# Kernel tuning notes

Hardware: AMD Instinct MI355X
Metric: run time of the kernel (lower is better)

Reference implementation:

```python
import jax, jax.numpy as jnp
import numpy as np

D_MODEL = 1024
NUM_HEADS = 16
HEAD_DIM = D_MODEL // NUM_HEADS


def setup_inputs() -> dict:
    key = jax.random.key(0)
    ks = jax.random.split(key, 5)
    x = jax.random.normal(ks[0], (4, 2048, D_MODEL), dtype=jnp.float32)
    # xavier_uniform with gain=0.1 for square (D,D) weights: limit = 0.1*sqrt(6/(D+D))
    limit = 0.1 * np.sqrt(6.0 / (2 * D_MODEL))
    def w(k):
        return jax.random.uniform(k, (D_MODEL, D_MODEL), jnp.float32, -limit, limit)
    return {
        "x": x,
        "W_q": w(ks[1]), "b_q": jnp.zeros((D_MODEL,), jnp.float32),
        "W_k": w(ks[2]), "b_k": jnp.zeros((D_MODEL,), jnp.float32),
        "W_v": w(ks[3]), "b_v": jnp.zeros((D_MODEL,), jnp.float32),
        "W_o": w(ks[4]), "b_o": jnp.zeros((D_MODEL,), jnp.float32),
    }


def reference(x, W_q, b_q, W_k, b_k, W_v, b_v, W_o, b_o):
    B, S, D = x.shape
    H, Hd = NUM_HEADS, HEAD_DIM
    # Linear: x @ W^T + b (torch nn.Linear convention); weights here are (out, in)
    def proj(W, b):
        y = jnp.einsum('bsd,ed->bse', x, W) + b
        return y.reshape(B, S, H, Hd).transpose(0, 2, 1, 3)  # [B,H,S,Hd]
    Q = proj(W_q, b_q)
    K = proj(W_k, b_k)
    V = proj(W_v, b_v)
    scale = 1.0 / np.sqrt(Hd).astype(np.float32)
    scores = jnp.einsum('bhqd,bhkd->bhqk', Q, K) * scale  # [B,H,S,S]
    attn = jax.nn.softmax(scores, axis=-1)
    ctx = jnp.einsum('bhqk,bhkd->bhqd', attn, V)
    ctx = ctx.transpose(0, 2, 1, 3).reshape(B, S, D)
    out = jnp.einsum('bsd,ed->bse', ctx, W_o) + b_o
    return out
```

## Files before the change

### kernel.cpp

```cpp
#include <hip/hip_runtime.h>
#include <math.h>

#define B_  4
#define S_  2048
#define D_  1024
#define H_  16
#define HD_ 64
#define M_  (B_*S_)

typedef short short8 __attribute__((ext_vector_type(8)));
typedef float f32x4 __attribute__((ext_vector_type(4)));

#define MFMA16(a,b,c) __builtin_amdgcn_mfma_f32_16x16x32_bf16(a, b, c, 0, 0, 0)

#if __has_builtin(__builtin_amdgcn_exp2f)
#define EXP2(x) __builtin_amdgcn_exp2f(x)
#else
#define EXP2(x) exp2f(x)
#endif

__device__ __forceinline__ unsigned short f2bf(float f) {
    unsigned u = __float_as_uint(f);
    u = (u + 0x7FFF + ((u >> 16) & 1)) >> 16;
    return (unsigned short)u;
}

__device__ __forceinline__ unsigned pack_bf16(float a, float b) {
#if __has_builtin(__builtin_amdgcn_cvt_pk_bf16_f32)
    typedef __bf16 bf2 __attribute__((ext_vector_type(2)));
    bf2 v = __builtin_amdgcn_cvt_pk_bf16_f32(a, b);
    unsigned r;
    __builtin_memcpy(&r, &v, 4);
    return r;
#else
    unsigned ua = __float_as_uint(a), ub = __float_as_uint(b);
    ua += 0x7FFFu + ((ua >> 16) & 1u);
    ub += 0x7FFFu + ((ub >> 16) & 1u);
    return __builtin_amdgcn_perm(ub, ua, 0x07060302u);
#endif
}

__device__ __forceinline__ void async_copy16(const void* g, void* l) {
    __builtin_amdgcn_global_load_lds(
        (const __attribute__((address_space(1))) void*)g,
        (__attribute__((address_space(3))) void*)l, 16, 0, 0);
}

__global__ __launch_bounds__(256) void cvt_all(
    const float* __restrict__ x,
    const float* __restrict__ w0, const float* __restrict__ w1,
    const float* __restrict__ w2, const float* __restrict__ w3,
    unsigned short* __restrict__ xb, unsigned short* __restrict__ wb)
{
    size_t i = ((size_t)blockIdx.x * 256 + threadIdx.x) * 4;
    const float* src; unsigned short* dst;
    if (i < (size_t)M_ * D_) {
        src = x + i; dst = xb + i;
    } else {
        size_t j = i - (size_t)M_ * D_;
        int z = (int)(j >> 20);
        const float* w = (z == 0) ? w0 : (z == 1) ? w1 : (z == 2) ? w2 : w3;
        src = w + (j & ((size_t)D_ * D_ - 1)); dst = wb + j;
    }
    float4 v = *(const float4*)src;
    uint2 o;
    o.x = pack_bf16(v.x, v.y);
    o.y = pack_bf16(v.z, v.w);
    *(uint2*)dst = o;
}

__global__ __launch_bounds__(512, 2) void qkv8(
    const unsigned short* __restrict__ A,
    const unsigned short* __restrict__ W,
    const float* __restrict__ bq, const float* __restrict__ bk,
    const float* __restrict__ bv,
    unsigned short* __restrict__ Qo, unsigned short* __restrict__ Ko,
    unsigned short* __restrict__ Vo)
{
    __shared__ unsigned short As[2][256 * 64];
    __shared__ unsigned short Ws[2][256 * 64];
    const int K = D_;
    int tid = threadIdx.x;
    int w = tid >> 6, lane = tid & 63;
    int quad = lane >> 4, l16 = lane & 15;
    int r8 = lane >> 3, c8 = lane & 7;
    int cK = c8 ^ r8;
    int wm = w >> 2, wn = w & 3;

    int lin = blockIdx.x + 12 * blockIdx.y;
    int swz = (lin & 7) * 48 + (lin >> 3);
    int by = swz / 12, bx = swz % 12;
    int m0 = by * 256, n0 = bx * 256;
    int fl = l16 & 7;

    int z = n0 >> 10;
    const float* bias = (z == 0) ? bq : (z == 1) ? bk : bv;
    unsigned short* out = (z == 0) ? Qo : (z == 1) ? Ko : Vo;
    float cscale = (z == 0) ? 0.125f * 1.44269504088896f : 1.0f;

    f32x4 acc[8][4];
    #pragma unroll
    for (int i = 0; i < 8; ++i)
        #pragma unroll
        for (int j = 0; j < 4; ++j)
            acc[i][j] = (f32x4){0.f, 0.f, 0.f, 0.f};

    const unsigned short* Ag = A + (size_t)(m0 + w * 8 + r8) * K + cK * 8;
    const unsigned short* Wg = W + (size_t)(n0 + w * 8 + r8) * K + cK * 8;

    auto stageA = [&](int slot, int kt) {
        #pragma unroll
        for (int ii = 0; ii < 4; ++ii)
            async_copy16(Ag + (size_t)(ii * 64) * K + kt * 64,
                         &As[slot][(ii * 64 + w * 8) * 64]);
    };
    auto stageW = [&](int slot, int kt) {
        #pragma unroll
        for (int ii = 0; ii < 4; ++ii)
            async_copy16(Wg + (size_t)(ii * 64) * K + kt * 64,
                         &Ws[slot][(ii * 64 + w * 8) * 64]);
    };

    stageA(0, 0);
    stageW(0, 0);
    __syncthreads();

    #define RDA(cur, i, s) (*(const short8*)&As[cur][(wm * 128 + (i) * 16 + l16) * 64 + \
                             (((quad + (s) * 4) ^ fl) * 8)])
    #define RDB(cur, j, s) (*(const short8*)&Ws[cur][(wn * 64 + (j) * 16 + l16) * 64 + \
                             (((quad + (s) * 4) ^ fl) * 8)])

    for (int kt = 0; kt < 16; ++kt) {
        int cur = kt & 1;
        bool pre = (kt < 15);
        short8 a[4][2], b0[2][2], b1[2][2];

        #pragma unroll
        for (int i = 0; i < 4; ++i)
            #pragma unroll
            for (int s = 0; s < 2; ++s) a[i][s] = RDA(cur, i, s);
        #pragma unroll
        for (int j = 0; j < 2; ++j)
            #pragma unroll
            for (int s = 0; s < 2; ++s) b0[j][s] = RDB(cur, j, s);
        if (pre) stageA(cur ^ 1, kt + 1);
        __builtin_amdgcn_s_setprio(1);
        #pragma unroll
        for (int i = 0; i < 4; ++i)
            #pragma unroll
            for (int j = 0; j < 2; ++j)
                #pragma unroll
                for (int s = 0; s < 2; ++s)
                    acc[i][j] = MFMA16(a[i][s], b0[j][s], acc[i][j]);
        __builtin_amdgcn_s_setprio(0);
        __builtin_amdgcn_s_barrier();
        __builtin_amdgcn_sched_barrier(0);

        #pragma unroll
        for (int j = 0; j < 2; ++j)
            #pragma unroll
            for (int s = 0; s < 2; ++s) b1[j][s] = RDB(cur, j + 2, s);
        if (pre) stageW(cur ^ 1, kt + 1);
        __builtin_amdgcn_s_setprio(1);
        #pragma unroll
        for (int i = 0; i < 4; ++i)
            #pragma unroll
            for (int j = 0; j < 2; ++j)
                #pragma unroll
                for (int s = 0; s < 2; ++s)
                    acc[i][j + 2] = MFMA16(a[i][s], b1[j][s], acc[i][j + 2]);
        __builtin_amdgcn_s_setprio(0);
        __builtin_amdgcn_s_barrier();
        __builtin_amdgcn_sched_barrier(0);

        #pragma unroll
        for (int i = 0; i < 4; ++i)
            #pragma unroll
            for (int s = 0; s < 2; ++s) a[i][s] = RDA(cur, i + 4, s);
        __builtin_amdgcn_s_setprio(1);
        #pragma unroll
        for (int i = 0; i < 4; ++i)
            #pragma unroll
            for (int j = 0; j < 2; ++j)
                #pragma unroll
                for (int s = 0; s < 2; ++s)
                    acc[i + 4][j + 2] = MFMA16(a[i][s], b1[j][s], acc[i + 4][j + 2]);
        __builtin_amdgcn_s_setprio(0);
        __builtin_amdgcn_s_barrier();
        __builtin_amdgcn_sched_barrier(0);

        __builtin_amdgcn_s_setprio(1);
        #pragma unroll
        for (int i = 0; i < 4; ++i)
            #pragma unroll
            for (int j = 0; j < 2; ++j)
                #pragma unroll
                for (int s = 0; s < 2; ++s)
                    acc[i + 4][j] = MFMA16(a[i][s], b0[j][s], acc[i + 4][j]);
        __builtin_amdgcn_s_setprio(0);
        asm volatile("s_waitcnt vmcnt(0)" ::: "memory");
        __builtin_amdgcn_s_barrier();
        __builtin_amdgcn_sched_barrier(0);
    }
    #undef RDA
    #undef RDB

    #pragma unroll
    for (int i = 0; i < 8; ++i) {
        int mb = m0 + wm * 128 + i * 16 + quad * 4;
        #pragma unroll
        for (int j = 0; j < 4; ++j) {
            int n = n0 + wn * 64 + j * 16 + l16;
            int nn = n & 1023;
            float bn = bias[nn];
            int h = nn >> 6, hd = nn & 63;
            if (z != 2) {
                #pragma unroll
                for (int r = 0; r < 4; ++r) {
                    int m = mb + r;
                    int bb = m >> 11, s = m & (S_ - 1);
                    out[(((size_t)(bb * H_ + h)) * S_ + s) * HD_ + hd] =
                        f2bf((acc[i][j][r] + bn) * cscale);
                }
            } else {
                int bb = mb >> 11, s0 = mb & (S_ - 1);
                uint2 o;
                o.x = pack_bf16(acc[i][j][0] + bn, acc[i][j][1] + bn);
                o.y = pack_bf16(acc[i][j][2] + bn, acc[i][j][3] + bn);
                *(uint2*)&out[(((size_t)(bb * H_ + h)) * HD_ + hd) * S_ + s0] = o;
            }
        }
    }
}

__device__ __forceinline__ void gemm_body(
    const unsigned short* __restrict__ A, const unsigned short* __restrict__ W,
    const float* __restrict__ bias, void* __restrict__ out,
    int mode, float cscale, int bx, int by)
{
    __shared__ unsigned short As[128 * 64];
    __shared__ unsigned short Ws[128 * 64];
    const int K = D_;
    int tid = threadIdx.x;
    int w = tid >> 6, lane = tid & 63;
    int quad = lane >> 4, l16 = lane & 15;
    int r8 = lane >> 3, c8 = lane & 7;
    int cK = c8 ^ r8;
    int wm = w >> 2, wn = w & 3;
    int m0 = by * 128, n0 = bx * 128;
    int fl = l16 & 7;

    f32x4 acc[4][2];
    #pragma unroll
    for (int i = 0; i < 4; ++i)
        #pragma unroll
        for (int j = 0; j < 2; ++j)
            acc[i][j] = (f32x4){0.f, 0.f, 0.f, 0.f};

    const unsigned short* Ag = A + (size_t)(m0 + w * 8 + r8) * K + cK * 8;
    const unsigned short* Wg = W + (size_t)(n0 + w * 8 + r8) * K + cK * 8;

    for (int k0 = 0; k0 < K; k0 += 64) {
        __syncthreads();
        #pragma unroll
        for (int ii = 0; ii < 2; ++ii) {
            async_copy16(Ag + k0 + (size_t)ii * 64 * K, As + (ii * 64 + w * 8) * 64);
            async_copy16(Wg + k0 + (size_t)ii * 64 * K, Ws + (ii * 64 + w * 8) * 64);
        }
        __syncthreads();
        #pragma unroll
        for (int s = 0; s < 2; ++s) {
            int st = ((quad + s * 4) ^ fl) * 8;
            short8 a[4], b[2];
            #pragma unroll
            for (int i = 0; i < 4; ++i)
                a[i] = *(const short8*)&As[(wm * 64 + i * 16 + l16) * 64 + st];
            #pragma unroll
            for (int j = 0; j < 2; ++j)
                b[j] = *(const short8*)&Ws[(wn * 32 + j * 16 + l16) * 64 + st];
            #pragma unroll
            for (int i = 0; i < 4; ++i)
                #pragma unroll
                for (int j = 0; j < 2; ++j)
                    acc[i][j] = MFMA16(a[i], b[j], acc[i][j]);
        }
    }

    #pragma unroll
    for (int i = 0; i < 4; ++i) {
        int mb = m0 + wm * 64 + i * 16 + quad * 4;
        #pragma unroll
        for (int j = 0; j < 2; ++j) {
            int n = n0 + wn * 32 + j * 16 + l16;
            float bn = bias[n];
            if (mode == 0) {
                #pragma unroll
                for (int r = 0; r < 4; ++r)
                    ((float*)out)[(size_t)(mb + r) * D_ + n] = acc[i][j][r] + bn;
            } else if (mode == 1) {
                int h = n >> 6, hd = n & 63;
                #pragma unroll
                for (int r = 0; r < 4; ++r) {
                    int m = mb + r;
                    int bb = m >> 11, s = m & (S_ - 1);
                    ((unsigned short*)out)[(((size_t)(bb * H_ + h)) * S_ + s) * HD_ + hd] =
                        f2bf((acc[i][j][r] + bn) * cscale);
                }
            } else {
                int h = n >> 6, hd = n & 63;
                int bb = mb >> 11, s0 = mb & (S_ - 1);
                uint2 o;
                o.x = pack_bf16(acc[i][j][0] + bn, acc[i][j][1] + bn);
                o.y = pack_bf16(acc[i][j][2] + bn, acc[i][j][3] + bn);
                *(uint2*)&((unsigned short*)out)[(((size_t)(bb * H_ + h)) * HD_ + hd) * S_ + s0] = o;
            }
        }
    }
}

__global__ __launch_bounds__(512) void out_gemm(
    const unsigned short* __restrict__ A, const unsigned short* __restrict__ W,
    const float* __restrict__ bias, float* __restrict__ out)
{
    int lin = blockIdx.x + 8 * blockIdx.y;
    int swz = (lin & 7) * 64 + (lin >> 3);
    gemm_body(A, W, bias, out, 0, 1.0f, swz & 7, swz >> 3);
}

__global__ __launch_bounds__(512, 4) void attn_mfma(
    const unsigned short* __restrict__ Q, const unsigned short* __restrict__ K,
    const unsigned short* __restrict__ VT, unsigned short* __restrict__ ctx)
{
    __shared__ unsigned short Ks[3 * 64 * 64];
    __shared__ unsigned short VTs[3 * 64 * 64];
    __shared__ unsigned short QPs[256 * 64];

    int tid = threadIdx.x;
    int w = tid >> 6, lane = tid & 63;
    int quad = lane >> 4, l16 = lane & 15;
    int r8 = lane >> 3, c8 = lane & 7;
    int cK = c8 ^ r8;
    int fl  = l16 & 7;
    int fl2 = (l16 ^ (l16 >> 1)) & 7;
    int bh = blockIdx.x;
    int q0 = blockIdx.y * 256;

    const unsigned short* Qp = Q + ((size_t)bh * S_ + q0) * HD_;
    const unsigned short* Kp = K + (size_t)bh * S_ * HD_;
    const unsigned short* Vp = VT + (size_t)bh * HD_ * S_;

    int cQ = c8 ^ r8 ^ (r8 >> 1) ^ ((w & 1) * 4);
    #pragma unroll
    for (int ii = 0; ii < 4; ++ii)
        async_copy16(Qp + (size_t)(ii * 64 + w * 8 + r8) * HD_ + cQ * 8,
                     QPs + (ii * 64 + w * 8) * 64);
    #pragma unroll
    for (int t = 0; t < 2; ++t) {
        async_copy16(Kp + (size_t)(t * 64 + w * 8 + r8) * HD_ + cK * 8,
                     Ks + t * 4096 + (w * 8) * 64);
        async_copy16(Vp + (size_t)(w * 8 + r8) * S_ + t * 64 + cK * 8,
                     VTs + t * 4096 + (w * 8) * 64);
    }
    __syncthreads();

    short8 bq_[2][2];
    #pragma unroll
    for (int mt = 0; mt < 2; ++mt)
        #pragma unroll
        for (int s = 0; s < 2; ++s)
            bq_[mt][s] = *(const short8*)&QPs[(w * 32 + mt * 16 + l16) * 64 +
                                              (((quad + s * 4) ^ fl2) * 8)];

    f32x4 O[2][4];
    float lsum[2] = {0.f, 0.f};
    #pragma unroll
    for (int mt = 0; mt < 2; ++mt)
        #pragma unroll
        for (int nt = 0; nt < 4; ++nt) O[mt][nt] = (f32x4){0.f, 0.f, 0.f, 0.f};

    const int NT = S_ / 64;
    for (int kt = 0; kt < NT; ++kt) {
        if (kt + 2 < NT) {
            int nb = ((kt + 2) % 3) * 4096;
            async_copy16(Kp + (size_t)((kt + 2) * 64 + w * 8 + r8) * HD_ + cK * 8,
                         Ks + nb + (w * 8) * 64);
            async_copy16(Vp + (size_t)(w * 8 + r8) * S_ + (kt + 2) * 64 + cK * 8,
                         VTs + nb + (w * 8) * 64);
        }
        const unsigned short* ks  = Ks + (kt % 3) * 4096;
        const unsigned short* vts = VTs + (kt % 3) * 4096;

        f32x4 sc[2][4];
        #pragma unroll
        for (int mt = 0; mt < 2; ++mt)
            #pragma unroll
            for (int nt = 0; nt < 4; ++nt) sc[mt][nt] = (f32x4){0.f, 0.f, 0.f, 0.f};
        #pragma unroll
        for (int s = 0; s < 2; ++s) {
            int stk = ((quad + s * 4) ^ fl) * 8;
            #pragma unroll
            for (int nt = 0; nt < 4; ++nt) {
                short8 ak = *(const short8*)&ks[(nt * 16 + l16) * 64 + stk];
                sc[0][nt] = MFMA16(ak, bq_[0][s], sc[0][nt]);
                sc[1][nt] = MFMA16(ak, bq_[1][s], sc[1][nt]);
            }
        }

        #pragma unroll
        for (int mt = 0; mt < 2; ++mt) {
            #pragma unroll
            for (int nt = 0; nt < 4; ++nt) {
                float p0 = EXP2(sc[mt][nt][0]);
                float p1 = EXP2(sc[mt][nt][1]);
                float p2 = EXP2(sc[mt][nt][2]);
                float p3 = EXP2(sc[mt][nt][3]);
                lsum[mt] += (p0 + p1) + (p2 + p3);
                uint2 pk;
                pk.x = pack_bf16(p0, p1);
                pk.y = pack_bf16(p2, p3);
                int addr = (w * 32 + mt * 16 + l16) * 64 +
                           (((nt * 2 + (quad >> 1)) ^ fl2) * 8) + (quad & 1) * 4;
                *(uint2*)&QPs[addr] = pk;
            }
        }

        #pragma unroll
        for (int s = 0; s < 2; ++s) {
            int stp = ((quad + s * 4) ^ fl2) * 8;
            int stv = ((quad + s * 4) ^ fl) * 8;
            short8 pa0 = *(const short8*)&QPs[(w * 32 + l16) * 64 + stp];
            short8 pa1 = *(const short8*)&QPs[(w * 32 + 16 + l16) * 64 + stp];
            #pragma unroll
            for (int nt = 0; nt < 4; ++nt) {
                short8 bv_ = *(const short8*)&vts[(nt * 16 + l16) * 64 + stv];
                O[0][nt] = MFMA16(pa0, bv_, O[0][nt]);
                O[1][nt] = MFMA16(pa1, bv_, O[1][nt]);
            }
        }

        if (kt + 2 < NT) asm volatile("s_waitcnt vmcnt(2)" ::: "memory");
        else             asm volatile("s_waitcnt vmcnt(0)" ::: "memory");
        __builtin_amdgcn_s_barrier();
        __builtin_amdgcn_sched_barrier(0);
    }

    float linv[2];
    #pragma unroll
    for (int mt = 0; mt < 2; ++mt) {
        float l = lsum[mt];
        l += __shfl_xor(l, 16);
        l += __shfl_xor(l, 32);
        linv[mt] = 1.0f / l;
    }

    int b = bh >> 4, h = bh & (H_ - 1);
    #pragma unroll
    for (int mt = 0; mt < 2; ++mt)
        #pragma unroll
        for (int r = 0; r < 4; ++r) {
            float inv = __shfl(linv[mt], quad * 4 + r, 64);
            int q = q0 + w * 32 + mt * 16 + quad * 4 + r;
            size_t base = ((size_t)(b * S_) + q) * D_ + h * HD_;
            #pragma unroll
            for (int nt = 0; nt < 4; ++nt)
                ctx[base + nt * 16 + l16] = f2bf(O[mt][nt][r] * inv);
        }
}

extern "C" void kernel_launch(void* const* d_in, const int* in_sizes, int n_in,
                              void* d_out, int out_size, void* d_ws, size_t ws_size,
                              hipStream_t stream) {
    const float* x  = (const float*)d_in[0];
    const float* Wq = (const float*)d_in[1];
    const float* bq = (const float*)d_in[2];
    const float* Wk = (const float*)d_in[3];
    const float* bk = (const float*)d_in[4];
    const float* Wv = (const float*)d_in[5];
    const float* bv = (const float*)d_in[6];
    const float* Wo = (const float*)d_in[7];
    const float* bo = (const float*)d_in[8];

    unsigned short* xb  = (unsigned short*)d_ws;
    unsigned short* wb  = xb + (size_t)M_ * D_;
    unsigned short* Qb  = wb + (size_t)4 * D_ * D_;
    unsigned short* Kb  = Qb + (size_t)M_ * D_;
    unsigned short* VTb = Kb + (size_t)M_ * D_;
    unsigned short* ctb = VTb + (size_t)M_ * D_;

    int cvt_blocks = (M_ * D_ + 4 * D_ * D_) / 1024;
    cvt_all<<<cvt_blocks, 256, 0, stream>>>(x, Wq, Wk, Wv, Wo, xb, wb);

    qkv8<<<dim3(3 * D_ / 256, M_ / 256), 512, 0, stream>>>(
        xb, wb, bq, bk, bv, Qb, Kb, VTb);

    attn_mfma<<<dim3(B_ * H_, S_ / 256), 512, 0, stream>>>(Qb, Kb, VTb, ctb);

    out_gemm<<<dim3(D_ / 128, M_ / 128), 512, 0, stream>>>(
        ctb, wb + (size_t)3 * D_ * D_, bo, (float*)d_out);
}
```

Measured before the change: 268.0 us.

## Split QKV GEMM prefetch into half-tiles and double-buffer output GEMM

The QKV GEMM now issues its next-tile async loads in quarter chunks spread across the four MFMA phases. Each chunk uses partial vmcnt waits, so the end-of-iteration vmcnt(0) stall goes away and the setprio hints are dropped. The output-projection GEMM gets double-buffered LDS with a one-tile prefetch, replacing its two syncthreads per k-step, and its launch bounds now request 4 blocks per CU. The intent is to overlap global-to-LDS traffic with MFMA work in both GEMMs. The cost is doubled LDS in out_gemm, which may limit occupancy, and the fine-grained wait counts are fragile to get right.

```diff
diff --git a/kernel.cpp b/kernel.cpp
--- a/kernel.cpp
+++ b/kernel.cpp
@@ -45,6 +45,10 @@
         (const __attribute__((address_space(1))) void*)g,
         (__attribute__((address_space(3))) void*)l, 16, 0, 0);
 }
+
+#define VMW(n) asm volatile("s_waitcnt vmcnt(" #n ")" ::: "memory")
+#define BARS() do { __builtin_amdgcn_s_barrier(); \
+                    __builtin_amdgcn_sched_barrier(0); } while (0)
 
 __global__ __launch_bounds__(256) void cvt_all(
     const float* __restrict__ x,
@@ -69,7 +73,7 @@
     *(uint2*)dst = o;
 }
 
-__global__ __launch_bounds__(512, 2) void qkv8(
+__global__ __launch_bounds__(512, 2) void qkv256(
     const unsigned short* __restrict__ A,
     const unsigned short* __restrict__ W,
     const float* __restrict__ bq, const float* __restrict__ bk,
@@ -86,14 +90,14 @@
     int r8 = lane >> 3, c8 = lane & 7;
     int cK = c8 ^ r8;
     int wm = w >> 2, wn = w & 3;
+    int fl = l16 & 7;
 
     int lin = blockIdx.x + 12 * blockIdx.y;
     int swz = (lin & 7) * 48 + (lin >> 3);
     int by = swz / 12, bx = swz % 12;
     int m0 = by * 256, n0 = bx * 256;
-    int fl = l16 & 7;
-
-    int z = n0 >> 10;
+
+    int z = bx >> 2;
     const float* bias = (z == 0) ? bq : (z == 1) ? bk : bv;
     unsigned short* out = (z == 0) ? Qo : (z == 1) ? Ko : Vo;
     float cscale = (z == 0) ? 0.125f * 1.44269504088896f : 1.0f;
@@ -105,46 +109,49 @@
         for (int j = 0; j < 4; ++j)
             acc[i][j] = (f32x4){0.f, 0.f, 0.f, 0.f};
 
-    const unsigned short* Ag = A + (size_t)(m0 + w * 8 + r8) * K + cK * 8;
-    const unsigned short* Wg = W + (size_t)(n0 + w * 8 + r8) * K + cK * 8;
-
-    auto stageA = [&](int slot, int kt) {
-        #pragma unroll
-        for (int ii = 0; ii < 4; ++ii)
-            async_copy16(Ag + (size_t)(ii * 64) * K + kt * 64,
-                         &As[slot][(ii * 64 + w * 8) * 64]);
+    const unsigned short* Ag = A + (size_t)(m0 + r8) * K + cK * 8;
+    const unsigned short* Wg = W + (size_t)(n0 + r8) * K + cK * 8;
+
+    auto stA = [&](int slot, int kt, int h) {
+        #pragma unroll
+        for (int ii = 0; ii < 2; ++ii) {
+            int rb = ii * 128 + h * 64 + w * 8;
+            async_copy16(Ag + (size_t)rb * K + kt * 64, &As[slot][rb * 64]);
+        }
     };
-    auto stageW = [&](int slot, int kt) {
-        #pragma unroll
-        for (int ii = 0; ii < 4; ++ii)
-            async_copy16(Wg + (size_t)(ii * 64) * K + kt * 64,
-                         &Ws[slot][(ii * 64 + w * 8) * 64]);
+    auto stB = [&](int slot, int kt, int h) {
+        #pragma unroll
+        for (int ii = 0; ii < 2; ++ii) {
+            int rb = (ii * 2 + (w >> 2)) * 64 + h * 32 + (w & 3) * 8;
+            async_copy16(Wg + (size_t)rb * K + kt * 64, &Ws[slot][rb * 64]);
+        }
     };
 
-    stageA(0, 0);
-    stageW(0, 0);
-    __syncthreads();
-
-    #define RDA(cur, i, s) (*(const short8*)&As[cur][(wm * 128 + (i) * 16 + l16) * 64 + \
-                             (((quad + (s) * 4) ^ fl) * 8)])
-    #define RDB(cur, j, s) (*(const short8*)&Ws[cur][(wn * 64 + (j) * 16 + l16) * 64 + \
-                             (((quad + (s) * 4) ^ fl) * 8)])
-
-    for (int kt = 0; kt < 16; ++kt) {
-        int cur = kt & 1;
-        bool pre = (kt < 15);
+    stA(0, 0, 0); stB(0, 0, 0); stB(0, 0, 1); stA(0, 0, 1);
+    VMW(4);
+    BARS();
+
+    #define RD_A(i, off, s) (*(const short8*)&As[cur][(wm * 128 + (off) + (i) * 16 + l16) * 64 + \
+                              (((quad + (s) * 4) ^ fl) * 8)])
+    #define RD_B(j, off, s) (*(const short8*)&Ws[cur][(wn * 64 + (off) + (j) * 16 + l16) * 64 + \
+                              (((quad + (s) * 4) ^ fl) * 8)])
+
+    const int NT = K / 64;
+    for (int kt = 0; kt < NT; ++kt) {
+        int cur = kt & 1, nxt = cur ^ 1;
+        bool pre = (kt + 1 < NT);
         short8 a[4][2], b0[2][2], b1[2][2];
 
         #pragma unroll
         for (int i = 0; i < 4; ++i)
             #pragma unroll
-            for (int s = 0; s < 2; ++s) a[i][s] = RDA(cur, i, s);
+            for (int s = 0; s < 2; ++s) a[i][s] = RD_A(i, 0, s);
         #pragma unroll
         for (int j = 0; j < 2; ++j)
             #pragma unroll
-            for (int s = 0; s < 2; ++s) b0[j][s] = RDB(cur, j, s);
-        if (pre) stageA(cur ^ 1, kt + 1);
-        __builtin_amdgcn_s_setprio(1);
+            for (int s = 0; s < 2; ++s) b0[j][s] = RD_B(j, 0, s);
+        if (pre) { stA(nxt, kt + 1, 0); VMW(4); } else VMW(2);
+        BARS();
         #pragma unroll
         for (int i = 0; i < 4; ++i)
             #pragma unroll
@@ -152,16 +159,13 @@
                 #pragma unroll
                 for (int s = 0; s < 2; ++s)
                     acc[i][j] = MFMA16(a[i][s], b0[j][s], acc[i][j]);
-        __builtin_amdgcn_s_setprio(0);
-        __builtin_amdgcn_s_barrier();
-        __builtin_amdgcn_sched_barrier(0);
 
         #pragma unroll
         for (int j = 0; j < 2; ++j)
             #pragma unroll
-            for (int s = 0; s < 2; ++s) b1[j][s] = RDB(cur, j + 2, s);
-        if (pre) stageW(cur ^ 1, kt + 1);
-        __builtin_amdgcn_s_setprio(1);
+            for (int s = 0; s < 2; ++s) b1[j][s] = RD_B(j, 32, s);
+        if (pre) { stB(nxt, kt + 1, 0); VMW(4); } else VMW(0);
+        BARS();
         #pragma unroll
         for (int i = 0; i < 4; ++i)
             #pragma unroll
@@ -169,15 +173,13 @@
                 #pragma unroll
                 for (int s = 0; s < 2; ++s)
                     acc[i][j + 2] = MFMA16(a[i][s], b1[j][s], acc[i][j + 2]);
-        __builtin_amdgcn_s_setprio(0);
-        __builtin_amdgcn_s_barrier();
-        __builtin_amdgcn_sched_barrier(0);
-
-        #pragma unroll
-        for (int i = 0; i < 4; ++i)
-            #pragma unroll
-            for (int s = 0; s < 2; ++s) a[i][s] = RDA(cur, i + 4, s);
-        __builtin_amdgcn_s_setprio(1);
+
+        #pragma unroll
+        for (int i = 0; i < 4; ++i)
+            #pragma unroll
+            for (int s = 0; s < 2; ++s) a[i][s] = RD_A(i, 64, s);
+        if (pre) stB(nxt, kt + 1, 1);
+        BARS();
         #pragma unroll
         for (int i = 0; i < 4; ++i)
             #pragma unroll
@@ -185,11 +187,9 @@
                 #pragma unroll
                 for (int s = 0; s < 2; ++s)
                     acc[i + 4][j + 2] = MFMA16(a[i][s], b1[j][s], acc[i + 4][j + 2]);
-        __builtin_amdgcn_s_setprio(0);
-        __builtin_amdgcn_s_barrier();
-        __builtin_amdgcn_sched_barrier(0);
-
-        __builtin_amdgcn_s_setprio(1);
+
+        if (pre) { stA(nxt, kt + 1, 1); VMW(4); }
+        BARS();
         #pragma unroll
         for (int i = 0; i < 4; ++i)
             #pragma unroll
@@ -197,36 +197,35 @@
                 #pragma unroll
                 for (int s = 0; s < 2; ++s)
                     acc[i + 4][j] = MFMA16(a[i][s], b0[j][s], acc[i + 4][j]);
-        __builtin_amdgcn_s_setprio(0);
-        asm volatile("s_waitcnt vmcnt(0)" ::: "memory");
-        __builtin_amdgcn_s_barrier();
-        __builtin_amdgcn_sched_barrier(0);
-    }
-    #undef RDA
-    #undef RDB
-
-    #pragma unroll
-    for (int i = 0; i < 8; ++i) {
-        int mb = m0 + wm * 128 + i * 16 + quad * 4;
+    }
+    #undef RD_A
+    #undef RD_B
+
+    #pragma unroll
+    for (int ih = 0; ih < 2; ++ih)
+    #pragma unroll
+    for (int i = 0; i < 4; ++i) {
+        int mb = m0 + wm * 128 + ih * 64 + i * 16 + quad * 4;
         #pragma unroll
         for (int j = 0; j < 4; ++j) {
             int n = n0 + wn * 64 + j * 16 + l16;
             int nn = n & 1023;
             float bn = bias[nn];
             int h = nn >> 6, hd = nn & 63;
+            f32x4 v = acc[ih * 4 + i][j];
             if (z != 2) {
                 #pragma unroll
                 for (int r = 0; r < 4; ++r) {
                     int m = mb + r;
                     int bb = m >> 11, s = m & (S_ - 1);
                     out[(((size_t)(bb * H_ + h)) * S_ + s) * HD_ + hd] =
-                        f2bf((acc[i][j][r] + bn) * cscale);
+                        f2bf((v[r] + bn) * cscale);
                 }
             } else {
                 int bb = mb >> 11, s0 = mb & (S_ - 1);
                 uint2 o;
-                o.x = pack_bf16(acc[i][j][0] + bn, acc[i][j][1] + bn);
-                o.y = pack_bf16(acc[i][j][2] + bn, acc[i][j][3] + bn);
+                o.x = pack_bf16(v[0] + bn, v[1] + bn);
+                o.y = pack_bf16(v[2] + bn, v[3] + bn);
                 *(uint2*)&out[(((size_t)(bb * H_ + h)) * HD_ + hd) * S_ + s0] = o;
             }
         }
@@ -238,8 +237,8 @@
     const float* __restrict__ bias, void* __restrict__ out,
     int mode, float cscale, int bx, int by)
 {
-    __shared__ unsigned short As[128 * 64];
-    __shared__ unsigned short Ws[128 * 64];
+    __shared__ unsigned short As[2][128 * 64];
+    __shared__ unsigned short Ws[2][128 * 64];
     const int K = D_;
     int tid = threadIdx.x;
     int w = tid >> 6, lane = tid & 63;
@@ -257,33 +256,47 @@
         for (int j = 0; j < 2; ++j)
             acc[i][j] = (f32x4){0.f, 0.f, 0.f, 0.f};
 
-    const unsigned short* Ag = A + (size_t)(m0 + w * 8 + r8) * K + cK * 8;
-    const unsigned short* Wg = W + (size_t)(n0 + w * 8 + r8) * K + cK * 8;
-
-    for (int k0 = 0; k0 < K; k0 += 64) {
-        __syncthreads();
+    const unsigned short* Ag = A + (size_t)(m0 + w * 16 + r8) * K + cK * 8;
+    const unsigned short* Wg = W + (size_t)(n0 + w * 16 + r8) * K + cK * 8;
+
+    auto stage = [&](int slot, int kt) {
         #pragma unroll
         for (int ii = 0; ii < 2; ++ii) {
-            async_copy16(Ag + k0 + (size_t)ii * 64 * K, As + (ii * 64 + w * 8) * 64);
-            async_copy16(Wg + k0 + (size_t)ii * 64 * K, Ws + (ii * 64 + w * 8) * 64);
-        }
-        __syncthreads();
+            async_copy16(Ag + (size_t)(ii * 8) * K + kt * 64,
+                         &As[slot][(w * 16 + ii * 8) * 64]);
+            async_copy16(Wg + (size_t)(ii * 8) * K + kt * 64,
+                         &Ws[slot][(w * 16 + ii * 8) * 64]);
+        }
+    };
+
+    stage(0, 0);
+    __syncthreads();
+
+    const int NT = K / 64;
+    for (int kt = 0; kt < NT; ++kt) {
+        int cur = kt & 1;
+        if (kt + 1 < NT) stage(cur ^ 1, kt + 1);
+
         #pragma unroll
         for (int s = 0; s < 2; ++s) {
             int st = ((quad + s * 4) ^ fl) * 8;
             short8 a[4], b[2];
             #pragma unroll
             for (int i = 0; i < 4; ++i)
-                a[i] = *(const short8*)&As[(wm * 64 + i * 16 + l16) * 64 + st];
+                a[i] = *(const short8*)&As[cur][(wm * 64 + i * 16 + l16) * 64 + st];
             #pragma unroll
             for (int j = 0; j < 2; ++j)
-                b[j] = *(const short8*)&Ws[(wn * 32 + j * 16 + l16) * 64 + st];
+                b[j] = *(const short8*)&Ws[cur][(wn * 32 + j * 16 + l16) * 64 + st];
             #pragma unroll
             for (int i = 0; i < 4; ++i)
                 #pragma unroll
                 for (int j = 0; j < 2; ++j)
                     acc[i][j] = MFMA16(a[i], b[j], acc[i][j]);
         }
+
+        asm volatile("s_waitcnt vmcnt(0)" ::: "memory");
+        __builtin_amdgcn_s_barrier();
+        __builtin_amdgcn_sched_barrier(0);
     }
 
     #pragma unroll
@@ -297,28 +310,12 @@
                 #pragma unroll
                 for (int r = 0; r < 4; ++r)
                     ((float*)out)[(size_t)(mb + r) * D_ + n] = acc[i][j][r] + bn;
-            } else if (mode == 1) {
-                int h = n >> 6, hd = n & 63;
-                #pragma unroll
-                for (int r = 0; r < 4; ++r) {
-                    int m = mb + r;
-                    int bb = m >> 11, s = m & (S_ - 1);
-                    ((unsigned short*)out)[(((size_t)(bb * H_ + h)) * S_ + s) * HD_ + hd] =
-                        f2bf((acc[i][j][r] + bn) * cscale);
-                }
-            } else {
-                int h = n >> 6, hd = n & 63;
-                int bb = mb >> 11, s0 = mb & (S_ - 1);
-                uint2 o;
-                o.x = pack_bf16(acc[i][j][0] + bn, acc[i][j][1] + bn);
-                o.y = pack_bf16(acc[i][j][2] + bn, acc[i][j][3] + bn);
-                *(uint2*)&((unsigned short*)out)[(((size_t)(bb * H_ + h)) * HD_ + hd) * S_ + s0] = o;
             }
         }
     }
 }
 
-__global__ __launch_bounds__(512) void out_gemm(
+__global__ __launch_bounds__(512, 4) void out_gemm(
     const unsigned short* __restrict__ A, const unsigned short* __restrict__ W,
     const float* __restrict__ bias, float* __restrict__ out)
 {
@@ -490,7 +487,7 @@
     int cvt_blocks = (M_ * D_ + 4 * D_ * D_) / 1024;
     cvt_all<<<cvt_blocks, 256, 0, stream>>>(x, Wq, Wk, Wv, Wo, xb, wb);
 
-    qkv8<<<dim3(3 * D_ / 256, M_ / 256), 512, 0, stream>>>(
+    qkv256<<<dim3(12, 32), 512, 0, stream>>>(
         xb, wb, bq, bk, bv, Qb, Kb, VTb);
 
     attn_mfma<<<dim3(B_ * H_, S_ / 256), 512, 0, stream>>>(Qb, Kb, VTb, ctb);
```

After: 269.1 us. Within noise of the previous version (+0.4%).
